# Optimization experiments

Measured on AMD Instinct MI355X. Metric: run time of the kernel, lower is better.

The kernel has to match this reference:

```python
import jax, jax.numpy as jnp
import numpy as np

B, S, D, H, E, K = 4, 1024, 1024, 4096, 8, 2


def setup_inputs() -> dict:
    key = jax.random.key(0)
    k1, k2, k3, k4 = jax.random.split(key, 4)
    x = jax.random.normal(k1, (B, S, D), dtype=jnp.float32)
    # expert params: two-layer MLP per expert, stacked along expert axis
    W1 = jax.random.normal(k2, (E, D, H), dtype=jnp.float32) * 0.02
    b1 = jnp.zeros((E, H), dtype=jnp.float32)
    W2 = jax.random.normal(k3, (E, H, D), dtype=jnp.float32) * 0.02
    b2 = jnp.zeros((E, D), dtype=jnp.float32)
    # hash-router assignments: k expert ids per token (stands in for HashRouter output)
    assign = jax.random.randint(k4, (B, S, K), 0, E, dtype=jnp.int64)
    return {"x": x, "W1": W1, "b1": b1, "W2": W2, "b2": b2, "assign": assign, "k": K}


def reference(x, W1, b1, W2, b2, assign, k):
    E_ = W1.shape[0]
    # mask[b,s,e] = 1 if expert e appears in assign[b,s,:] (matches (assign==idx).any(-1),
    # so a duplicated assignment contributes once, exactly like the torch loop)
    mask = (assign[..., None] == jnp.arange(E_)[None, None, None, :]).any(axis=-2)
    # run every token through every expert, then mask-combine (dense MoE reference)
    h = jax.nn.relu(jnp.einsum('bsd,edh->bseh', x, W1) + b1)      # [B,S,E,H]
    y = jnp.einsum('bseh,ehd->bsed', h, W2) + b2                  # [B,S,E,D]
    out = jnp.einsum('bsed,bse->bsd', y, mask.astype(x.dtype))
    return out / k
```

## Files before the change

### kernel.cpp

```cpp
#include <hip/hip_runtime.h>
#include <hip/hip_bf16.h>

#define DIM_D 1024
#define DIM_H 4096
#define NUM_E 8
#define NUM_TOK 4096
#define MAXROWS 8320

typedef __attribute__((ext_vector_type(8))) short short8;
typedef __attribute__((ext_vector_type(4))) float floatx4;

__device__ __forceinline__ unsigned short f2bf(float f) {
  union { float f; unsigned int u; } v; v.f = f;
  unsigned int r = v.u + 0x7fffu + ((v.u >> 16) & 1u);
  return (unsigned short)(r >> 16);
}

__device__ __forceinline__ void async_copy16(const void* g, void* l) {
  __builtin_amdgcn_global_load_lds(
      (__attribute__((address_space(1))) unsigned int*)(g),
      (__attribute__((address_space(3))) unsigned int*)(l), 16, 0, 0);
}

__global__ __launch_bounds__(256) void route_scan(
    const int* __restrict__ assign, int* __restrict__ counts,
    int* __restrict__ offsets, int* __restrict__ tok2row) {
  __shared__ int hist[256][NUM_E];
  __shared__ int base[NUM_E];
  const int tid = threadIdx.x;
  const int t0 = tid * 16;
#pragma unroll
  for (int e = 0; e < NUM_E; e++) hist[tid][e] = 0;
  const int4* ap = (const int4*)(assign + t0 * 2);
  for (int i = 0; i < 8; i++) {
    int4 v = ap[i];
    hist[tid][v.x]++; if (v.y != v.x) hist[tid][v.y]++;
    hist[tid][v.z]++; if (v.w != v.z) hist[tid][v.w]++;
  }
  __syncthreads();
  if (tid < NUM_E) {
    int acc = 0;
    for (int i = 0; i < 256; i++) { int v = hist[i][tid]; hist[i][tid] = acc; acc += v; }
    base[tid] = acc;
  }
  __syncthreads();
  if (tid == 0) {
    int acc = 0;
    for (int e = 0; e < NUM_E; e++) {
      int tot = base[e];
      counts[e] = tot; offsets[e] = acc; base[e] = acc; acc += tot;
    }
  }
  __syncthreads();
#pragma unroll
  for (int e = 0; e < NUM_E; e++) hist[tid][e] += base[e];
  for (int i = 0; i < 8; i++) {
    int4 v = ap[i];
    int t = t0 + 2 * i;
    int4 o;
    o.x = hist[tid][v.x]++;
    o.y = (v.y != v.x) ? hist[tid][v.y]++ : -1;
    o.z = hist[tid][v.z]++;
    o.w = (v.w != v.z) ? hist[tid][v.w]++ : -1;
    *(int4*)(tok2row + 2 * t) = o;
  }
}

__global__ void gather_x(const float* __restrict__ x, const int* __restrict__ tok2row,
                         unsigned short* __restrict__ Xg) {
  int t = blockIdx.x;
  int r0 = tok2row[2 * t], r1 = tok2row[2 * t + 1];
  const float4* xv = (const float4*)(x + (size_t)t * DIM_D);
  float4 v0 = xv[threadIdx.x * 2];
  float4 v1 = xv[threadIdx.x * 2 + 1];
  unsigned short h[8];
  h[0] = f2bf(v0.x); h[1] = f2bf(v0.y); h[2] = f2bf(v0.z); h[3] = f2bf(v0.w);
  h[4] = f2bf(v1.x); h[5] = f2bf(v1.y); h[6] = f2bf(v1.z); h[7] = f2bf(v1.w);
  uint4 pack = *(uint4*)h;
  *(uint4*)(Xg + (size_t)r0 * DIM_D + threadIdx.x * 8) = pack;
  if (r1 >= 0)
    *(uint4*)(Xg + (size_t)r1 * DIM_D + threadIdx.x * 8) = pack;
}

__global__ __launch_bounds__(256) void transpose_cvt64(
    const float* __restrict__ W1, const float* __restrict__ W2,
    unsigned short* __restrict__ W1t, unsigned short* __restrict__ W2t) {
  __shared__ float tile[64 * 64];
  const int z = blockIdx.y;
  const int e = z >> 1, which = z & 1;
  const int R = which ? DIM_H : DIM_D;
  const int C = which ? DIM_D : DIM_H;
  const int nbx = C / 64;
  const int bx = blockIdx.x % nbx;
  const int by = blockIdx.x / nbx;
  const float* ip = (which ? W2 : W1) + (size_t)e * R * C + (size_t)(by * 64) * C + bx * 64;
  unsigned short* op = (which ? W2t : W1t) + (size_t)e * R * C + (size_t)(bx * 64) * R + by * 64;
  const int tid = threadIdx.x;

  {
    int chunk = tid & 15;
    int rb = tid >> 4;
#pragma unroll
    for (int p = 0; p < 4; p++) {
      int r = rb + p * 16;
      float4 v = *(const float4*)(ip + (size_t)r * C + chunk * 4);
      int slot = chunk ^ (r >> 3);
      *(float4*)&tile[r * 64 + slot * 4] = v;
    }
  }
  __syncthreads();
  {
    int s = tid & 7;
    int c0 = tid >> 3;
#pragma unroll
    for (int i = 0; i < 2; i++) {
      int c = c0 + i * 32;
      int ch = c >> 2, cl = c & 3;
      int base = ((ch ^ s) * 4) + cl;
      unsigned short h[8];
#pragma unroll
      for (int j = 0; j < 8; j++) {
        int r = 8 * s + j;
        h[j] = f2bf(tile[r * 64 + base]);
      }
      *(uint4*)(op + (size_t)c * R + 8 * s) = *(const uint4*)h;
    }
  }
}

template <int MODE, int KTOT>
__global__ __launch_bounds__(256) void moe_gemm(
    const unsigned short* __restrict__ Ain, const unsigned short* __restrict__ Bt,
    const float* __restrict__ bias, const int* __restrict__ counts,
    const int* __restrict__ offsets,
    unsigned short* __restrict__ Hout, float* __restrict__ Yout,
    int lda, int ldb, int N) {
  int e, half;
  if (MODE == 0) { e = blockIdx.z; half = 0; }
  else           { e = blockIdx.z >> 1; half = blockIdx.z & 1; }
  const int cnt = counts[e];
  int mt_, nt_;
  if (MODE == 0) {
    nt_ = (blockIdx.x & 7) | ((blockIdx.y & 3) << 3);
    mt_ = (blockIdx.x >> 3) | ((blockIdx.y >> 2) << 2);
  } else {
    nt_ = blockIdx.x; mt_ = blockIdx.y;
  }
  const int m0 = mt_ * 128;
  if (m0 >= cnt) return;
  const int n0 = nt_ * 128;
  const int rowbase = offsets[e];
  const unsigned short* A = Ain + (size_t)half * KTOT;

  __shared__ unsigned short sh[2 * 128 * 64];
  unsigned short* As = sh;
  unsigned short* Bs = sh + 128 * 64;

  const int tid = threadIdx.x;
  const int w = tid >> 6;
  const int lane = tid & 63;
  const int l15 = lane & 15, l4 = lane >> 4;
  const int wm = w >> 1, wn = w & 1;
  const int lrow = lane >> 3, lslot = lane & 7;
  const int lchunk = lslot ^ lrow;

  const unsigned short* gA[4]; const unsigned short* gB[4];
  void* dA[4]; void* dB[4];
  const unsigned short* Bbase = Bt + (size_t)e * N * ldb + (size_t)half * KTOT;
#pragma unroll
  for (int p = 0; p < 4; p++) {
    int rw = p * 32 + w * 8;
    gA[p] = A + (size_t)(rowbase + m0 + rw + lrow) * lda + lchunk * 8;
    gB[p] = Bbase + (size_t)(n0 + rw + lrow) * ldb + lchunk * 8;
    dA[p] = (char*)As + rw * 128;
    dB[p] = (char*)Bs + rw * 128;
  }

  floatx4 acc[4][4];
#pragma unroll
  for (int i = 0; i < 4; i++)
#pragma unroll
    for (int j = 0; j < 4; j++) acc[i][j] = (floatx4){0.f, 0.f, 0.f, 0.f};

  int arow[4], brow[4], sl[2];
  sl[0] = ((l4 + 0) ^ (l15 & 7)) * 8;
  sl[1] = ((l4 + 4) ^ (l15 & 7)) * 8;
#pragma unroll
  for (int mt = 0; mt < 4; mt++) arow[mt] = (wm * 64 + mt * 16 + l15) * 64;
#pragma unroll
  for (int nt = 0; nt < 4; nt++) brow[nt] = (wn * 64 + nt * 16 + l15) * 64;

  for (int k0 = 0; k0 < KTOT; k0 += 64) {
    __syncthreads();
#pragma unroll
    for (int p = 0; p < 4; p++) async_copy16(gA[p], dA[p]);
#pragma unroll
    for (int p = 0; p < 4; p++) async_copy16(gB[p], dB[p]);
#pragma unroll
    for (int p = 0; p < 4; p++) { gA[p] += 64; gB[p] += 64; }
    __syncthreads();
#pragma unroll
    for (int s = 0; s < 2; s++) {
      short8 a[4], b[4];
#pragma unroll
      for (int mt = 0; mt < 4; mt++) a[mt] = *(const short8*)(As + arow[mt] + sl[s]);
#pragma unroll
      for (int nt = 0; nt < 4; nt++) b[nt] = *(const short8*)(Bs + brow[nt] + sl[s]);
#pragma unroll
      for (int mt = 0; mt < 4; mt++)
#pragma unroll
        for (int nt = 0; nt < 4; nt++)
          acc[mt][nt] = __builtin_amdgcn_mfma_f32_16x16x32_bf16(a[mt], b[nt], acc[mt][nt], 0, 0, 0);
    }
  }

  __syncthreads();
  float* sbuf = (float*)sh + w * 1088;
  const bool addb = (MODE == 0) || (half == 0);
  const float* be = bias + (size_t)e * N + n0 + wn * 64;
  float* yplane = (MODE == 1) ? (Yout + (size_t)half * MAXROWS * N) : nullptr;
#pragma unroll
  for (int mt = 0; mt < 4; mt++) {
#pragma unroll
    for (int nt = 0; nt < 4; nt++) {
      float bv = addb ? be[nt * 16 + l15] : 0.f;
#pragma unroll
      for (int r = 0; r < 4; r++) {
        float v = acc[mt][nt][r] + bv;
        if (MODE == 0) v = fmaxf(v, 0.f);
        sbuf[(l4 * 4 + r) * 68 + nt * 16 + l15] = v;
      }
    }
    __asm__ __volatile__("s_waitcnt lgkmcnt(0)" ::: "memory");
#pragma unroll
    for (int pass = 0; pass < 4; pass++) {
      int row = pass * 4 + l4;
      int col4 = l15 * 4;
      int gm = m0 + wm * 64 + mt * 16 + row;
      float4 v = *(const float4*)&sbuf[row * 68 + col4];
      if (gm < cnt) {
        size_t off = (size_t)(rowbase + gm) * N + n0 + wn * 64 + col4;
        if (MODE == 0) {
          ushort4 h;
          h.x = f2bf(v.x); h.y = f2bf(v.y); h.z = f2bf(v.z); h.w = f2bf(v.w);
          *(ushort4*)(Hout + off) = h;
        } else {
          *(float4*)(yplane + off) = v;
        }
      }
    }
    __asm__ __volatile__("s_waitcnt lgkmcnt(0)" ::: "memory");
  }
}

__global__ void combine_k(const float* __restrict__ Yg, const int* __restrict__ tok2row,
                          const int* __restrict__ kptr, float* __restrict__ out) {
  int t = blockIdx.x;
  int r0 = tok2row[2 * t], r1 = tok2row[2 * t + 1];
  float invk = 1.0f / (float)kptr[0];
  int d = threadIdx.x * 4;
  const size_t plane = (size_t)MAXROWS * DIM_D;
  float4 v = *(const float4*)(Yg + (size_t)r0 * DIM_D + d);
  float4 u = *(const float4*)(Yg + plane + (size_t)r0 * DIM_D + d);
  v.x += u.x; v.y += u.y; v.z += u.z; v.w += u.w;
  if (r1 >= 0) {
    float4 a = *(const float4*)(Yg + (size_t)r1 * DIM_D + d);
    float4 b = *(const float4*)(Yg + plane + (size_t)r1 * DIM_D + d);
    v.x += a.x + b.x; v.y += a.y + b.y; v.z += a.z + b.z; v.w += a.w + b.w;
  }
  float4 o; o.x = v.x * invk; o.y = v.y * invk; o.z = v.z * invk; o.w = v.w * invk;
  *(float4*)(out + (size_t)t * DIM_D + d) = o;
}


extern "C" void kernel_launch(void* const* d_in, const int* in_sizes, int n_in,
                              void* d_out, int out_size, void* d_ws, size_t ws_size,
                              hipStream_t stream) {
  const float* x = (const float*)d_in[0];
  const float* W1 = (const float*)d_in[1];
  const float* b1 = (const float*)d_in[2];
  const float* W2 = (const float*)d_in[3];
  const float* b2 = (const float*)d_in[4];
  const int* assign = (const int*)d_in[5];
  const int* kptr = (const int*)d_in[6];
  float* out = (float*)d_out;

  char* p = (char*)d_ws;
  int* counts = (int*)p; p += 256;
  int* offsets = (int*)p; p += 256;
  int* tok2row = (int*)p; p += NUM_TOK * 2 * 4;
  unsigned short* W1t = (unsigned short*)p; p += (size_t)NUM_E * DIM_D * DIM_H * 2;
  unsigned short* Xg = (unsigned short*)p; p += (size_t)MAXROWS * DIM_D * 2;
  unsigned short* Hg = (unsigned short*)p; p += (size_t)MAXROWS * DIM_H * 2;
  unsigned short* W2t = (unsigned short*)p; p += (size_t)NUM_E * DIM_D * DIM_H * 2;
  float* Yg = (float*)W1t;

  route_scan<<<1, 256, 0, stream>>>(assign, counts, offsets, tok2row);
  gather_x<<<NUM_TOK, 128, 0, stream>>>(x, tok2row, Xg);

  transpose_cvt64<<<dim3(1024, 16), 256, 0, stream>>>(W1, W2, W1t, W2t);

  moe_gemm<0, DIM_D><<<dim3(32, 32, NUM_E), 256, 0, stream>>>(
      Xg, W1t, b1, counts, offsets, Hg, nullptr, DIM_D, DIM_D, DIM_H);
  moe_gemm<1, DIM_H / 2><<<dim3(8, 32, NUM_E * 2), 256, 0, stream>>>(
      Hg, W2t, b2, counts, offsets, nullptr, Yg, DIM_H, DIM_H, DIM_D);

  combine_k<<<NUM_TOK, 256, 0, stream>>>(Yg, tok2row, kptr, out);
}
```

Measured before the change: 547.5 us.

## Batch transpose tiles per block with register prefetch and remap GEMM block order

The weight transpose/convert kernel now processes eight 64x64 tiles per block. It double-buffers shared memory and prefetches the next tile into registers while the current one is written out, which amortizes launch overhead and hides global load latency. The MoE GEMM launches switch to a 1D grid with an explicit mapping that groups N-tiles by XCD (l&7) to improve L2 locality of weight reads. This adds register pressure and depends on the assumed round-robin dispatch of blocks across XCDs.

```diff
diff --git a/kernel.cpp b/kernel.cpp
--- a/kernel.cpp
+++ b/kernel.cpp
@@ -82,47 +82,59 @@
     *(uint4*)(Xg + (size_t)r1 * DIM_D + threadIdx.x * 8) = pack;
 }
 
+#define TPT 8
 __global__ __launch_bounds__(256) void transpose_cvt64(
     const float* __restrict__ W1, const float* __restrict__ W2,
     unsigned short* __restrict__ W1t, unsigned short* __restrict__ W2t) {
-  __shared__ float tile[64 * 64];
-  const int z = blockIdx.y;
+  __shared__ float tile[2][64 * 64];
+  const int tid = threadIdx.x;
+  const int gbase = blockIdx.x * TPT;
+  const int z = gbase >> 10;
+  const int m0 = gbase & 1023;
   const int e = z >> 1, which = z & 1;
   const int R = which ? DIM_H : DIM_D;
   const int C = which ? DIM_D : DIM_H;
   const int nbx = C / 64;
-  const int bx = blockIdx.x % nbx;
-  const int by = blockIdx.x / nbx;
-  const float* ip = (which ? W2 : W1) + (size_t)e * R * C + (size_t)(by * 64) * C + bx * 64;
-  unsigned short* op = (which ? W2t : W1t) + (size_t)e * R * C + (size_t)(bx * 64) * R + by * 64;
-  const int tid = threadIdx.x;
-
-  {
-    int chunk = tid & 15;
-    int rb = tid >> 4;
+  const float* in0 = (which ? W2 : W1) + (size_t)e * R * C;
+  unsigned short* out0 = (which ? W2t : W1t) + (size_t)e * R * C;
+
+  const int chunk = tid & 15, rb = tid >> 4;
+  const int s = tid & 7, c0 = tid >> 3;
+  const int by = m0 / nbx;
+  const int bx0 = m0 % nbx;
+  const float* ipbase = in0 + (size_t)(by * 64) * C + (size_t)bx0 * 64;
+
+  float4 rA[4], rB[4];
+#pragma unroll
+  for (int p = 0; p < 4; p++)
+    rA[p] = *(const float4*)(ipbase + (size_t)(rb + p * 16) * C + chunk * 4);
+
+#pragma unroll
+  for (int i = 0; i < TPT; i++) {
+    float* buf = tile[i & 1];
 #pragma unroll
     for (int p = 0; p < 4; p++) {
       int r = rb + p * 16;
-      float4 v = *(const float4*)(ip + (size_t)r * C + chunk * 4);
       int slot = chunk ^ (r >> 3);
-      *(float4*)&tile[r * 64 + slot * 4] = v;
-    }
-  }
-  __syncthreads();
-  {
-    int s = tid & 7;
-    int c0 = tid >> 3;
-#pragma unroll
-    for (int i = 0; i < 2; i++) {
-      int c = c0 + i * 32;
-      int ch = c >> 2, cl = c & 3;
-      int base = ((ch ^ s) * 4) + cl;
+      *(float4*)&buf[r * 64 + slot * 4] = (i & 1) ? rB[p] : rA[p];
+    }
+    if (i + 1 < TPT) {
+      const float* ip = ipbase + (size_t)(i + 1) * 64;
+#pragma unroll
+      for (int p = 0; p < 4; p++) {
+        float4 v = *(const float4*)(ip + (size_t)(rb + p * 16) * C + chunk * 4);
+        if (i & 1) rA[p] = v; else rB[p] = v;
+      }
+    }
+    __syncthreads();
+    unsigned short* op = out0 + (size_t)((bx0 + i) * 64) * R + by * 64;
+#pragma unroll
+    for (int ii = 0; ii < 2; ii++) {
+      int c = c0 + ii * 32;
+      int base = (((c >> 2) ^ s) * 4) + (c & 3);
       unsigned short h[8];
 #pragma unroll
-      for (int j = 0; j < 8; j++) {
-        int r = 8 * s + j;
-        h[j] = f2bf(tile[r * 64 + base]);
-      }
+      for (int j = 0; j < 8; j++) h[j] = f2bf(buf[(8 * s + j) * 64 + base]);
       *(uint4*)(op + (size_t)c * R + 8 * s) = *(const uint4*)h;
     }
   }
@@ -141,10 +153,14 @@
   const int cnt = counts[e];
   int mt_, nt_;
   if (MODE == 0) {
-    nt_ = (blockIdx.x & 7) | ((blockIdx.y & 3) << 3);
-    mt_ = (blockIdx.x >> 3) | ((blockIdx.y >> 2) << 2);
+    int l = blockIdx.x;
+    int xcd = l & 7, sIdx = l >> 3;
+    nt_ = xcd * 4 + (sIdx & 3);
+    mt_ = sIdx >> 2;
   } else {
-    nt_ = blockIdx.x; mt_ = blockIdx.y;
+    int l = blockIdx.x;
+    nt_ = l & 7;
+    mt_ = l >> 3;
   }
   const int m0 = mt_ * 128;
   if (m0 >= cnt) return;
@@ -298,11 +314,11 @@
   route_scan<<<1, 256, 0, stream>>>(assign, counts, offsets, tok2row);
   gather_x<<<NUM_TOK, 128, 0, stream>>>(x, tok2row, Xg);
 
-  transpose_cvt64<<<dim3(1024, 16), 256, 0, stream>>>(W1, W2, W1t, W2t);
-
-  moe_gemm<0, DIM_D><<<dim3(32, 32, NUM_E), 256, 0, stream>>>(
+  transpose_cvt64<<<16384 / TPT, 256, 0, stream>>>(W1, W2, W1t, W2t);
+
+  moe_gemm<0, DIM_D><<<dim3(1024, 1, NUM_E), 256, 0, stream>>>(
       Xg, W1t, b1, counts, offsets, Hg, nullptr, DIM_D, DIM_D, DIM_H);
-  moe_gemm<1, DIM_H / 2><<<dim3(8, 32, NUM_E * 2), 256, 0, stream>>>(
+  moe_gemm<1, DIM_H / 2><<<dim3(256, 1, NUM_E * 2), 256, 0, stream>>>(
       Hg, W2t, b2, counts, offsets, nullptr, Yg, DIM_H, DIM_H, DIM_D);
 
   combine_k<<<NUM_TOK, 256, 0, stream>>>(Yg, tok2row, kptr, out);
```

Result: no change. 549.9 us (+0.4%).
